# Kernel tuning notes

Hardware: AMD Instinct MI355X
Metric: run time of the kernel (lower is better)

## Reference

```python
import jax, jax.numpy as jnp
import numpy as np

GROUPS = 8
EPS = 1e-5
NUM_HEADS = 8


def group_norm(x, gamma, beta):
    # x: [B, C, N]; GroupNorm over (C//G, N) per group, per sample (torch semantics)
    B, C, N = x.shape
    xg = x.reshape(B, GROUPS, (C // GROUPS) * N)
    mean = xg.mean(axis=-1, keepdims=True)
    var = xg.var(axis=-1, keepdims=True)
    xn = ((xg - mean) * jax.lax.rsqrt(var + EPS)).reshape(B, C, N)
    return xn * gamma[None, :, None] + beta[None, :, None]


def setup_inputs() -> dict:
    key = jax.random.key(0)
    ks = jax.random.split(key, 6)
    B, N, C = 4, 2048, 512
    s = 0.02
    return {
        "x": jax.random.normal(ks[0], (B, N, C), jnp.float32),
        "pe": jax.random.normal(ks[1], (B, N, C), jnp.float32),
        "qkv_w": jax.random.normal(ks[2], (3 * C, C), jnp.float32) * s,
        "proj_w": jax.random.normal(ks[3], (C, C), jnp.float32) * s,
        "proj_b": jnp.zeros((C,), jnp.float32),
        "conv1_w": jax.random.normal(ks[4], (C, C), jnp.float32) * s,
        "conv1_b": jnp.zeros((C,), jnp.float32),
        "gn1_g": jnp.ones((C,), jnp.float32),
        "gn1_b": jnp.zeros((C,), jnp.float32),
        "conv2_w": jax.random.normal(ks[5], (C, C), jnp.float32) * s,
        "conv2_b": jnp.zeros((C,), jnp.float32),
        "gn2_g": jnp.ones((C,), jnp.float32),
        "gn2_b": jnp.zeros((C,), jnp.float32),
    }


def reference(x, pe, qkv_w, proj_w, proj_b, conv1_w, conv1_b, gn1_g, gn1_b,
              conv2_w, conv2_b, gn2_g, gn2_b):
    B, N, C = x.shape
    H = NUM_HEADS
    D = C // H
    scale = D ** -0.5

    pe_t = pe.transpose(0, 2, 1)  # [B, C, N]
    # Conv1d(kernel=1) == per-position linear over channels
    p1 = group_norm(jnp.einsum('oc,bcn->bon', conv1_w, pe_t) + conv1_b[None, :, None], gn1_g, gn1_b)
    p2 = group_norm(jnp.einsum('oc,bcn->bon', conv2_w, pe_t) + conv2_b[None, :, None], gn2_g, gn2_b)
    pe_1 = p1.transpose(0, 2, 1)                 # [B, N, C]
    pe_attn = jax.nn.sigmoid(jnp.einsum('bnc,bcm->bnm', pe_1, p2))  # [B, N, N]

    qkv = (x @ qkv_w.T).reshape(B, N, 3, H, D).transpose(2, 0, 3, 1, 4)  # [3, B, H, N, D]
    q, k, v = qkv[0], qkv[1], qkv[2]

    attn = jnp.einsum('bhnd,bhmd->bhnm', q, k) * scale
    attn = attn * pe_attn[:, None, :, :]
    attn = jax.nn.softmax(attn, axis=-1)

    out = jnp.einsum('bhnm,bhmd->bhnd', attn, v)          # [B, H, N, D]
    out = out.transpose(0, 2, 1, 3).reshape(B, N, C)
    return out @ proj_w.T + proj_b
```

## Files before the change

### kernel.cpp

```cpp
#include <hip/hip_runtime.h>
#include <hip/hip_bf16.h>

typedef __attribute__((ext_vector_type(8))) short bf16x8;
typedef __attribute__((ext_vector_type(4))) float f32x4;

__device__ __forceinline__ float bfu2f(unsigned int u) {
    return __uint_as_float(u << 16);
}
__device__ __forceinline__ unsigned short f2bfu(float f) {
    unsigned int u = __float_as_uint(f);
    u += 0x7fffu + ((u >> 16) & 1u);
    return (unsigned short)(u >> 16);
}

__global__ __launch_bounds__(256) void cvt2(const float* __restrict__ s0, unsigned short* __restrict__ d0,
                                            const float* __restrict__ s1, unsigned short* __restrict__ d1) {
    int i = blockIdx.x * 256 + threadIdx.x;
    const int stride = gridDim.x * 256;
    for (; i < 1048576; i += stride) {
        float4 v = reinterpret_cast<const float4*>(s0)[i];
        ushort4 o;
        o.x = f2bfu(v.x); o.y = f2bfu(v.y); o.z = f2bfu(v.z); o.w = f2bfu(v.w);
        reinterpret_cast<ushort4*>(d0)[i] = o;
        float4 u = reinterpret_cast<const float4*>(s1)[i];
        ushort4 p;
        p.x = f2bfu(u.x); p.y = f2bfu(u.y); p.z = f2bfu(u.z); p.w = f2bfu(u.w);
        reinterpret_cast<ushort4*>(d1)[i] = p;
    }
}

__global__ __launch_bounds__(256) void cvtw(const float* __restrict__ s0, unsigned short* __restrict__ d0,
                                            const float* __restrict__ s1, unsigned short* __restrict__ d1,
                                            const float* __restrict__ s2, unsigned short* __restrict__ d2,
                                            const float* __restrict__ s3, unsigned short* __restrict__ d3) {
    int i = blockIdx.x * 256 + threadIdx.x;
    const int stride = gridDim.x * 256;
    for (; i < 393216; i += stride) {
        const float* s; unsigned short* d; int j;
        if (i < 196608)      { s = s0; d = d0; j = i; }
        else if (i < 262144) { s = s1; d = d1; j = i - 196608; }
        else if (i < 327680) { s = s2; d = d2; j = i - 262144; }
        else                 { s = s3; d = d3; j = i - 327680; }
        float4 v = reinterpret_cast<const float4*>(s)[j];
        ushort4 o;
        o.x = f2bfu(v.x); o.y = f2bfu(v.y); o.z = f2bfu(v.z); o.w = f2bfu(v.w);
        reinterpret_cast<ushort4*>(d)[j] = o;
    }
}

template <int EPI>
__global__ __launch_bounds__(256) void gemm_nt(
    const unsigned short* __restrict__ A, const unsigned short* __restrict__ B,
    void* __restrict__ C0, void* __restrict__ C1, void* __restrict__ C2,
    const float* __restrict__ bias, int K, long sA, long sB, long sC) {
    __shared__ unsigned short As[2][128 * 32];
    __shared__ unsigned short Bs[2][128 * 32];
    const int tid = threadIdx.x;
    const int l = tid & 63, w = tid >> 6;
    const int wr = w >> 1, wc = w & 1, lr = l & 15, lh = l >> 4;
    const int m0 = blockIdx.y * 128, n0 = blockIdx.x * 128;
    A += (size_t)blockIdx.z * sA;
    B += (size_t)blockIdx.z * sB;
    f32x4 acc[4][4] = {};

    const int srow = l >> 2, sslot = l & 3;
    auto stage = [&](int bufi, int k0) {
#pragma unroll
        for (int i = 0; i < 2; i++) {
            const int row = w * 32 + i * 16 + srow;
            const int cs = (sslot ^ (row & 3)) * 8;
            const int ldsoff = (w * 32 + i * 16) * 32;
            __builtin_amdgcn_global_load_lds(
                (const __attribute__((address_space(1))) void*)(A + (size_t)(m0 + row) * K + k0 + cs),
                (__attribute__((address_space(3))) void*)&As[bufi][ldsoff], 16, 0, 0);
            __builtin_amdgcn_global_load_lds(
                (const __attribute__((address_space(1))) void*)(B + (size_t)(n0 + row) * K + k0 + cs),
                (__attribute__((address_space(3))) void*)&Bs[bufi][ldsoff], 16, 0, 0);
        }
    };

    const int nks = K >> 5;
    stage(0, 0);
    asm volatile("s_waitcnt vmcnt(0)" ::: "memory");
    __builtin_amdgcn_s_barrier();
    __builtin_amdgcn_sched_barrier(0);

    const int colA = (lh ^ (lr & 3)) << 3;
    for (int ks = 0; ks < nks; ks++) {
        const int cur = ks & 1;
        if (ks + 1 < nks) stage(cur ^ 1, (ks + 1) << 5);
        bf16x8 af[4], bfr[4];
#pragma unroll
        for (int i = 0; i < 4; i++)
            af[i] = *reinterpret_cast<const bf16x8*>(&As[cur][(wr * 64 + i * 16 + lr) * 32 + colA]);
#pragma unroll
        for (int i = 0; i < 4; i++)
            bfr[i] = *reinterpret_cast<const bf16x8*>(&Bs[cur][(wc * 64 + i * 16 + lr) * 32 + colA]);
        __builtin_amdgcn_s_setprio(1);
#pragma unroll
        for (int mi = 0; mi < 4; mi++)
#pragma unroll
            for (int ni = 0; ni < 4; ni++)
                acc[mi][ni] = __builtin_amdgcn_mfma_f32_16x16x32_bf16(af[mi], bfr[ni], acc[mi][ni], 0, 0, 0);
        __builtin_amdgcn_s_setprio(0);
        if (ks + 1 < nks) {
            asm volatile("s_waitcnt vmcnt(0) lgkmcnt(0)" ::: "memory");
            __builtin_amdgcn_s_barrier();
            __builtin_amdgcn_sched_barrier(0);
        }
    }

#pragma unroll
    for (int mi = 0; mi < 4; mi++) {
#pragma unroll
        for (int ni = 0; ni < 4; ni++) {
#pragma unroll
            for (int r = 0; r < 4; r++) {
                const int row = m0 + wr * 64 + mi * 16 + lh * 4 + r;
                const int col = n0 + wc * 64 + ni * 16 + lr;
                float v = acc[mi][ni][r];
                if constexpr (EPI == 0) {
                    v += bias[col];
                    ((unsigned short*)C0)[(size_t)row * 512 + col] = f2bfu(v);
                } else if constexpr (EPI == 1) {
                    const int part = col >> 9, hh = (col >> 6) & 7, d = col & 63;
                    const int b = row >> 11, n = row & 2047;
                    const size_t bh = (size_t)(b * 8 + hh);
                    if (part == 0)
                        ((unsigned short*)C0)[(bh * 2048 + n) * 64 + d] = f2bfu(v * 0.1803368801111244f);
                    else if (part == 1)
                        ((unsigned short*)C1)[(bh * 2048 + n) * 64 + d] = f2bfu(v);
                    else
                        ((unsigned short*)C2)[(bh * 64 + d) * 2048 + n] = f2bfu(v);
                } else if constexpr (EPI == 2) {
                    const float sg = 1.0f / (1.0f + __expf(-v));
                    ((unsigned short*)C0)[(size_t)blockIdx.z * sC + (size_t)row * 2048 + col] = f2bfu(sg);
                } else {
                    ((float*)C0)[(size_t)row * 512 + col] = v + bias[col];
                }
            }
        }
    }
}

__global__ __launch_bounds__(256) void gn_stats_part(const unsigned short* __restrict__ c1,
                                                     const unsigned short* __restrict__ c2,
                                                     float* __restrict__ part) {
    const int bgc = blockIdx.x;
    const int b = bgc >> 6, g = (bgc >> 3) & 7, ch = bgc & 7;
    const int tid = threadIdx.x;
    const size_t base = ((size_t)b * 2048 + ch * 256) * 512 + g * 64;
    float s1 = 0.f, q1 = 0.f, s2 = 0.f, q2 = 0.f;
    for (int c = tid; c < 2048; c += 256) {
        const int n = c >> 3, i8 = (c & 7) * 8;
        const size_t off = base + (size_t)n * 512 + i8;
        uint4 v1 = *reinterpret_cast<const uint4*>(c1 + off);
        uint4 v2 = *reinterpret_cast<const uint4*>(c2 + off);
        unsigned int a1[4] = {v1.x, v1.y, v1.z, v1.w};
        unsigned int a2[4] = {v2.x, v2.y, v2.z, v2.w};
#pragma unroll
        for (int j = 0; j < 4; j++) {
            float x0 = bfu2f(a1[j] & 0xffffu), x1 = bfu2f(a1[j] >> 16);
            s1 += x0 + x1; q1 += x0 * x0 + x1 * x1;
            float y0 = bfu2f(a2[j] & 0xffffu), y1 = bfu2f(a2[j] >> 16);
            s2 += y0 + y1; q2 += y0 * y0 + y1 * y1;
        }
    }
#pragma unroll
    for (int off = 32; off >= 1; off >>= 1) {
        s1 += __shfl_down(s1, off); q1 += __shfl_down(q1, off);
        s2 += __shfl_down(s2, off); q2 += __shfl_down(q2, off);
    }
    __shared__ float red[4][4];
    if ((tid & 63) == 0) {
        const int wv = tid >> 6;
        red[0][wv] = s1; red[1][wv] = q1; red[2][wv] = s2; red[3][wv] = q2;
    }
    __syncthreads();
    if (tid == 0) {
        part[bgc * 4 + 0] = red[0][0] + red[0][1] + red[0][2] + red[0][3];
        part[bgc * 4 + 1] = red[1][0] + red[1][1] + red[1][2] + red[1][3];
        part[bgc * 4 + 2] = red[2][0] + red[2][1] + red[2][2] + red[2][3];
        part[bgc * 4 + 3] = red[3][0] + red[3][1] + red[3][2] + red[3][3];
    }
}

__global__ __launch_bounds__(256) void gn_apply(unsigned short* __restrict__ c1,
                                                unsigned short* __restrict__ c2,
                                                const float* __restrict__ part,
                                                const float* __restrict__ g1, const float* __restrict__ b1,
                                                const float* __restrict__ g2, const float* __restrict__ b2) {
    __shared__ float sst[32][4];
    const int tid = threadIdx.x;
    if (tid < 32) {
        float S1 = 0.f, Q1 = 0.f, S2 = 0.f, Q2 = 0.f;
        for (int ch = 0; ch < 8; ch++) {
            const float* p = part + ((tid << 3) + ch) * 4;
            S1 += p[0]; Q1 += p[1]; S2 += p[2]; Q2 += p[3];
        }
        const float inv = 1.0f / 131072.0f;
        float m1 = S1 * inv, m2 = S2 * inv;
        float v1 = fmaxf(Q1 * inv - m1 * m1, 0.f);
        float v2 = fmaxf(Q2 * inv - m2 * m2, 0.f);
        sst[tid][0] = m1;
        sst[tid][1] = rsqrtf(v1 + 1e-5f);
        sst[tid][2] = m2;
        sst[tid][3] = rsqrtf(v2 + 1e-5f);
    }
    __syncthreads();
    int i = blockIdx.x * 256 + tid;
    const int stride = gridDim.x * 256;
    for (; i < 524288; i += stride) {
        const size_t e = (size_t)i * 8;
        const int b = (int)(e >> 20);
        const int o = (int)(e & 511);
        const int g = o >> 6;
        const float* st = sst[(b << 3) + g];
        const float m1 = st[0], r1 = st[1], m2 = st[2], r2 = st[3];
        uint4 v1 = *reinterpret_cast<const uint4*>(c1 + e);
        uint4 v2 = *reinterpret_cast<const uint4*>(c2 + e);
        unsigned int a1[4] = {v1.x, v1.y, v1.z, v1.w};
        unsigned int a2[4] = {v2.x, v2.y, v2.z, v2.w};
        unsigned int o1[4], o2[4];
#pragma unroll
        for (int j = 0; j < 4; j++) {
            const int oo = o + j * 2;
            float x0 = (bfu2f(a1[j] & 0xffffu) - m1) * r1 * g1[oo] + b1[oo];
            float x1 = (bfu2f(a1[j] >> 16) - m1) * r1 * g1[oo + 1] + b1[oo + 1];
            o1[j] = (unsigned int)f2bfu(x0) | ((unsigned int)f2bfu(x1) << 16);
            float y0 = (bfu2f(a2[j] & 0xffffu) - m2) * r2 * g2[oo] + b2[oo];
            float y1 = (bfu2f(a2[j] >> 16) - m2) * r2 * g2[oo + 1] + b2[oo + 1];
            o2[j] = (unsigned int)f2bfu(y0) | ((unsigned int)f2bfu(y1) << 16);
        }
        uint4 w1; w1.x = o1[0]; w1.y = o1[1]; w1.z = o1[2]; w1.w = o1[3];
        uint4 w2; w2.x = o2[0]; w2.y = o2[1]; w2.z = o2[2]; w2.w = o2[3];
        *reinterpret_cast<uint4*>(c1 + e) = w1;
        *reinterpret_cast<uint4*>(c2 + e) = w2;
    }
}

__global__ __launch_bounds__(256, 4) void attn_fused(
    const unsigned short* __restrict__ qb, const unsigned short* __restrict__ kb,
    const unsigned short* __restrict__ vT, const unsigned short* __restrict__ pea,
    unsigned short* __restrict__ hbuf) {
    __shared__ unsigned short Ks[2][64 * 64];
    __shared__ unsigned short Vs[2][64 * 64];
    __shared__ unsigned short Pl[4][16 * 64];
    const int tid = threadIdx.x, l = tid & 63, w = tid >> 6;
    const int lr = l & 15, lh = l >> 4;
    const int bid = blockIdx.x;
    const int h = bid >> 7, rst = bid & 127, nt = rst & 31, b = rst >> 5;
    const size_t bh = (size_t)(b * 8 + h);
    const unsigned short* qp = qb + bh * 2048 * 64;
    const unsigned short* kp = kb + bh * 2048 * 64;
    const unsigned short* vp = vT + bh * 64 * 2048;
    const unsigned short* pep = pea + (size_t)b * 2048 * 2048;
    const int n0 = nt * 64;

    bf16x8 qf[2];
    qf[0] = *reinterpret_cast<const bf16x8*>(qp + (size_t)(n0 + 16 * w + lr) * 64 + lh * 8);
    qf[1] = *reinterpret_cast<const bf16x8*>(qp + (size_t)(n0 + 16 * w + lr) * 64 + 32 + lh * 8);

    const int swz = (lr & 7) << 4;
    const int colK0 = ((16 * lh) ^ swz) >> 1;
    const int colK1 = ((64 + 16 * lh) ^ swz) >> 1;

    const unsigned short* perp = pep + (size_t)(n0 + 16 * w + lr) * 2048;
    uint2 peR[4];
#pragma unroll
    for (int mf = 0; mf < 4; mf++)
        peR[mf] = *reinterpret_cast<const uint2*>(perp + 16 * mf + 4 * lh);

    f32x4 oacc[4] = {};
    float mrun = -1e30f, lrun = 0.f;

    const int srow = l >> 3, sslot = l & 7;
    auto stage_kv = [&](int bufi, int m0) {
#pragma unroll
        for (int i = 0; i < 2; i++) {
            const int row = w * 16 + i * 8 + srow;
            const int cs = (sslot ^ (row & 7)) * 8;
            const int ldsoff = (w * 16 + i * 8) * 64;
            __builtin_amdgcn_global_load_lds(
                (const __attribute__((address_space(1))) void*)(kp + (size_t)(m0 + row) * 64 + cs),
                (__attribute__((address_space(3))) void*)&Ks[bufi][ldsoff], 16, 0, 0);
            __builtin_amdgcn_global_load_lds(
                (const __attribute__((address_space(1))) void*)(vp + (size_t)row * 2048 + m0 + cs),
                (__attribute__((address_space(3))) void*)&Vs[bufi][ldsoff], 16, 0, 0);
        }
    };

    stage_kv(0, 0);
    asm volatile("s_waitcnt vmcnt(0)" ::: "memory");
    __builtin_amdgcn_s_barrier();
    __builtin_amdgcn_sched_barrier(0);

    for (int mt = 0; mt < 32; mt++) {
        const int cur = mt & 1;
        if (mt + 1 < 32) stage_kv(cur ^ 1, (mt + 1) * 64);
        const unsigned short* Kb = Ks[cur];
        const unsigned short* Vb = Vs[cur];

        f32x4 st[4] = {};
        __builtin_amdgcn_s_setprio(1);
#pragma unroll
        for (int mf = 0; mf < 4; mf++) {
            bf16x8 kf0 = *reinterpret_cast<const bf16x8*>(&Kb[(mf * 16 + lr) * 64 + colK0]);
            bf16x8 kf1 = *reinterpret_cast<const bf16x8*>(&Kb[(mf * 16 + lr) * 64 + colK1]);
            st[mf] = __builtin_amdgcn_mfma_f32_16x16x32_bf16(kf0, qf[0], st[mf], 0, 0, 0);
            st[mf] = __builtin_amdgcn_mfma_f32_16x16x32_bf16(kf1, qf[1], st[mf], 0, 0, 0);
        }
        __builtin_amdgcn_s_setprio(0);

        float p[4][4];
#pragma unroll
        for (int mf = 0; mf < 4; mf++) {
            p[mf][0] = st[mf][0] * bfu2f(peR[mf].x & 0xffffu);
            p[mf][1] = st[mf][1] * bfu2f(peR[mf].x >> 16);
            p[mf][2] = st[mf][2] * bfu2f(peR[mf].y & 0xffffu);
            p[mf][3] = st[mf][3] * bfu2f(peR[mf].y >> 16);
        }
        uint2 peN[4];
        if (mt + 1 < 32) {
            const unsigned short* pn = perp + (mt + 1) * 64;
#pragma unroll
            for (int mf = 0; mf < 4; mf++)
                peN[mf] = *reinterpret_cast<const uint2*>(pn + 16 * mf + 4 * lh);
        }
        float pm = fmaxf(p[0][0], p[0][1]);
        pm = fmaxf(fmaxf(pm, p[0][2]), p[0][3]);
#pragma unroll
        for (int mf = 1; mf < 4; mf++) {
            pm = fmaxf(fmaxf(pm, p[mf][0]), p[mf][1]);
            pm = fmaxf(fmaxf(pm, p[mf][2]), p[mf][3]);
        }
        pm = fmaxf(pm, __shfl_xor(pm, 16));
        pm = fmaxf(pm, __shfl_xor(pm, 32));
        if (__any(pm > mrun + 11.5416f)) {
            const float mnew = fmaxf(mrun, pm);
            const float fac = __builtin_amdgcn_exp2f(mrun - mnew);
            lrun *= fac;
#pragma unroll
            for (int df = 0; df < 4; df++)
#pragma unroll
                for (int r = 0; r < 4; r++) oacc[df][r] *= fac;
            mrun = mnew;
        }
        float ss = 0.f;
        unsigned int pk[8];
#pragma unroll
        for (int mf = 0; mf < 4; mf++) {
#pragma unroll
            for (int t = 0; t < 2; t++) {
                const float a = __builtin_amdgcn_exp2f(p[mf][2 * t] - mrun);
                const float c = __builtin_amdgcn_exp2f(p[mf][2 * t + 1] - mrun);
                unsigned int pkv;
                asm("v_cvt_pk_bf16_f32 %0, %1, %2" : "=v"(pkv) : "v"(a), "v"(c));
                pk[mf * 2 + t] = pkv;
                ss += a + c;
            }
        }
        ss += __shfl_xor(ss, 16);
        ss += __shfl_xor(ss, 32);
        lrun += ss;
        unsigned short* PlW = Pl[w];
        const int plswz = (lr & 7) << 4;
#pragma unroll
        for (int mf = 0; mf < 4; mf++)
#pragma unroll
            for (int t = 0; t < 2; t++) {
                const int cb = (mf * 32 + lh * 8 + 4 * t) ^ plswz;
                *reinterpret_cast<unsigned int*>(&PlW[lr * 64 + (cb >> 1)]) = pk[mf * 2 + t];
            }
        bf16x8 pb0 = *reinterpret_cast<const bf16x8*>(&PlW[lr * 64 + (((lh * 16) ^ plswz) >> 1)]);
        bf16x8 pb1 = *reinterpret_cast<const bf16x8*>(&PlW[lr * 64 + (((64 + lh * 16) ^ plswz) >> 1)]);
        __builtin_amdgcn_s_setprio(1);
#pragma unroll
        for (int df = 0; df < 4; df++) {
            bf16x8 vf0 = *reinterpret_cast<const bf16x8*>(&Vb[(df * 16 + lr) * 64 + colK0]);
            bf16x8 vf1 = *reinterpret_cast<const bf16x8*>(&Vb[(df * 16 + lr) * 64 + colK1]);
            oacc[df] = __builtin_amdgcn_mfma_f32_16x16x32_bf16(vf0, pb0, oacc[df], 0, 0, 0);
            oacc[df] = __builtin_amdgcn_mfma_f32_16x16x32_bf16(vf1, pb1, oacc[df], 0, 0, 0);
        }
        __builtin_amdgcn_s_setprio(0);
        if (mt + 1 < 32) {
            asm volatile("s_waitcnt vmcnt(0) lgkmcnt(0)" ::: "memory");
            __builtin_amdgcn_s_barrier();
            __builtin_amdgcn_sched_barrier(0);
#pragma unroll
            for (int mf = 0; mf < 4; mf++) peR[mf] = peN[mf];
        }
    }
    const float inv = 1.0f / lrun;
    const size_t base = ((size_t)b * 2048 + n0 + 16 * w + lr) * 512 + h * 64;
#pragma unroll
    for (int df = 0; df < 4; df++) {
#pragma unroll
        for (int t = 0; t < 2; t++) {
            const unsigned int ua = f2bfu(oacc[df][2 * t] * inv);
            const unsigned int uc = f2bfu(oacc[df][2 * t + 1] * inv);
            *reinterpret_cast<unsigned int*>(&hbuf[base + 16 * df + 4 * lh + 2 * t]) = ua | (uc << 16);
        }
    }
}

extern "C" void kernel_launch(void* const* d_in, const int* in_sizes, int n_in,
                              void* d_out, int out_size, void* d_ws, size_t ws_size,
                              hipStream_t stream) {
    const float* x       = (const float*)d_in[0];
    const float* pe      = (const float*)d_in[1];
    const float* qkv_w   = (const float*)d_in[2];
    const float* proj_w  = (const float*)d_in[3];
    const float* proj_b  = (const float*)d_in[4];
    const float* conv1_w = (const float*)d_in[5];
    const float* conv1_b = (const float*)d_in[6];
    const float* gn1_g   = (const float*)d_in[7];
    const float* gn1_b   = (const float*)d_in[8];
    const float* conv2_w = (const float*)d_in[9];
    const float* conv2_b = (const float*)d_in[10];
    const float* gn2_g   = (const float*)d_in[11];
    const float* gn2_b   = (const float*)d_in[12];
    float* out = (float*)d_out;

    char* ws = (char*)d_ws;
    size_t off = 0;
    auto alloc = [&](size_t bytes) -> void* {
        void* p = ws + off;
        off += (bytes + 255) & ~(size_t)255;
        return p;
    };
    unsigned short* xb     = (unsigned short*)alloc(8388608);
    unsigned short* peb    = (unsigned short*)alloc(8388608);
    unsigned short* qkvwb  = (unsigned short*)alloc(1572864);
    unsigned short* projwb = (unsigned short*)alloc(524288);
    unsigned short* w1b    = (unsigned short*)alloc(524288);
    unsigned short* w2b    = (unsigned short*)alloc(524288);
    unsigned short* c1b    = (unsigned short*)alloc(8388608);
    unsigned short* c2b    = (unsigned short*)alloc(8388608);
    unsigned short* qbuf   = (unsigned short*)alloc(8388608);
    unsigned short* kbuf   = (unsigned short*)alloc(8388608);
    unsigned short* vtb    = (unsigned short*)alloc(8388608);
    unsigned short* peatt  = (unsigned short*)alloc(33554432);
    unsigned short* hbuf   = (unsigned short*)alloc(8388608);
    float* part            = (float*)alloc(4096);

    dim3 blk(256);
    cvt2<<<1024, blk, 0, stream>>>(x, xb, pe, peb);
    cvtw<<<512, blk, 0, stream>>>(qkv_w, qkvwb, proj_w, projwb, conv1_w, w1b, conv2_w, w2b);

    gemm_nt<0><<<dim3(4, 64, 1), blk, 0, stream>>>(peb, w1b, c1b, nullptr, nullptr, conv1_b, 512, 0, 0, 0);
    gemm_nt<0><<<dim3(4, 64, 1), blk, 0, stream>>>(peb, w2b, c2b, nullptr, nullptr, conv2_b, 512, 0, 0, 0);
    gn_stats_part<<<256, blk, 0, stream>>>(c1b, c2b, part);
    gn_apply<<<1024, blk, 0, stream>>>(c1b, c2b, part, gn1_g, gn1_b, gn2_g, gn2_b);
    gemm_nt<1><<<dim3(12, 64, 1), blk, 0, stream>>>(xb, qkvwb, qbuf, kbuf, vtb, nullptr, 512, 0, 0, 0);
    gemm_nt<2><<<dim3(16, 16, 4), blk, 0, stream>>>(c1b, c2b, peatt, nullptr, nullptr, nullptr, 512,
                                                    1048576, 1048576, 4194304);
    attn_fused<<<dim3(1024, 1, 1), blk, 0, stream>>>(qbuf, kbuf, vtb, peatt, hbuf);
    gemm_nt<3><<<dim3(4, 64, 1), blk, 0, stream>>>(hbuf, projwb, out, nullptr, nullptr, proj_b, 512, 0, 0, 0);
}
```

Before: 232.5 us.

## Fuse conversion kernels, batch conv GEMMs, and compute GroupNorm stats in epilogue

Merges the activation and weight fp32-to-bf16 conversion kernels into one launch that also packs both conv biases into a contiguous workspace. The two conv1/conv2 GEMMs become a single launch using blockIdx.z, with the weights assumed adjacent in the workspace so sB=262144 selects the second. Each wave accumulates GroupNorm sum and sum-of-squares in the epilogue and atomically adds them into a zeroed buffer, which removes the separate stats pass over c1/c2. The cost is a memset, float atomics with nondeterministic summation order, and statistics taken from fp32 values before bf16 rounding.

Result: no change. 228.6 us (-1.7%).

```diff
diff --git a/kernel.cpp b/kernel.cpp
--- a/kernel.cpp
+++ b/kernel.cpp
@@ -13,38 +13,44 @@
     return (unsigned short)(u >> 16);
 }
 
-__global__ __launch_bounds__(256) void cvt2(const float* __restrict__ s0, unsigned short* __restrict__ d0,
-                                            const float* __restrict__ s1, unsigned short* __restrict__ d1) {
-    int i = blockIdx.x * 256 + threadIdx.x;
+__global__ __launch_bounds__(256) void cvt_all(
+    const float* __restrict__ x, unsigned short* __restrict__ xb,
+    const float* __restrict__ pe, unsigned short* __restrict__ peb,
+    const float* __restrict__ w0, unsigned short* __restrict__ d0,
+    const float* __restrict__ w1, unsigned short* __restrict__ d1,
+    const float* __restrict__ w2, unsigned short* __restrict__ d2,
+    const float* __restrict__ w3, unsigned short* __restrict__ d3,
+    const float* __restrict__ c1bias, const float* __restrict__ c2bias,
+    float* __restrict__ biasws) {
+    const int tid = threadIdx.x;
+    if (blockIdx.x == 0) {
+        if (tid < 128) ((float4*)biasws)[tid] = ((const float4*)c1bias)[tid];
+        else ((float4*)biasws)[tid] = ((const float4*)c2bias)[tid - 128];
+    }
+    int i = blockIdx.x * 256 + tid;
     const int stride = gridDim.x * 256;
-    for (; i < 1048576; i += stride) {
-        float4 v = reinterpret_cast<const float4*>(s0)[i];
-        ushort4 o;
-        o.x = f2bfu(v.x); o.y = f2bfu(v.y); o.z = f2bfu(v.z); o.w = f2bfu(v.w);
-        reinterpret_cast<ushort4*>(d0)[i] = o;
-        float4 u = reinterpret_cast<const float4*>(s1)[i];
-        ushort4 p;
-        p.x = f2bfu(u.x); p.y = f2bfu(u.y); p.z = f2bfu(u.z); p.w = f2bfu(u.w);
-        reinterpret_cast<ushort4*>(d1)[i] = p;
-    }
-}
-
-__global__ __launch_bounds__(256) void cvtw(const float* __restrict__ s0, unsigned short* __restrict__ d0,
-                                            const float* __restrict__ s1, unsigned short* __restrict__ d1,
-                                            const float* __restrict__ s2, unsigned short* __restrict__ d2,
-                                            const float* __restrict__ s3, unsigned short* __restrict__ d3) {
-    int i = blockIdx.x * 256 + threadIdx.x;
-    const int stride = gridDim.x * 256;
-    for (; i < 393216; i += stride) {
-        const float* s; unsigned short* d; int j;
-        if (i < 196608)      { s = s0; d = d0; j = i; }
-        else if (i < 262144) { s = s1; d = d1; j = i - 196608; }
-        else if (i < 327680) { s = s2; d = d2; j = i - 262144; }
-        else                 { s = s3; d = d3; j = i - 327680; }
-        float4 v = reinterpret_cast<const float4*>(s)[j];
-        ushort4 o;
-        o.x = f2bfu(v.x); o.y = f2bfu(v.y); o.z = f2bfu(v.z); o.w = f2bfu(v.w);
-        reinterpret_cast<ushort4*>(d)[j] = o;
+    for (; i < 1441792; i += stride) {
+        if (i < 1048576) {
+            float4 v = reinterpret_cast<const float4*>(x)[i];
+            ushort4 o;
+            o.x = f2bfu(v.x); o.y = f2bfu(v.y); o.z = f2bfu(v.z); o.w = f2bfu(v.w);
+            reinterpret_cast<ushort4*>(xb)[i] = o;
+            float4 u = reinterpret_cast<const float4*>(pe)[i];
+            ushort4 p;
+            p.x = f2bfu(u.x); p.y = f2bfu(u.y); p.z = f2bfu(u.z); p.w = f2bfu(u.w);
+            reinterpret_cast<ushort4*>(peb)[i] = p;
+        } else {
+            int j = i - 1048576;
+            const float* s; unsigned short* d;
+            if (j < 196608)      { s = w0; d = d0; }
+            else if (j < 262144) { s = w1; d = d1; j -= 196608; }
+            else if (j < 327680) { s = w2; d = d2; j -= 262144; }
+            else                 { s = w3; d = d3; j -= 327680; }
+            float4 v = reinterpret_cast<const float4*>(s)[j];
+            ushort4 o;
+            o.x = f2bfu(v.x); o.y = f2bfu(v.y); o.z = f2bfu(v.z); o.w = f2bfu(v.w);
+            reinterpret_cast<ushort4*>(d)[j] = o;
+        }
     }
 }
 
@@ -110,6 +116,7 @@
         }
     }
 
+    float sgn = 0.f, qgn = 0.f;
 #pragma unroll
     for (int mi = 0; mi < 4; mi++) {
 #pragma unroll
@@ -120,8 +127,9 @@
                 const int col = n0 + wc * 64 + ni * 16 + lr;
                 float v = acc[mi][ni][r];
                 if constexpr (EPI == 0) {
-                    v += bias[col];
-                    ((unsigned short*)C0)[(size_t)row * 512 + col] = f2bfu(v);
+                    v += bias[blockIdx.z * 512 + col];
+                    sgn += v; qgn += v * v;
+                    ((unsigned short*)C0)[(size_t)blockIdx.z * sC + (size_t)row * 512 + col] = f2bfu(v);
                 } else if constexpr (EPI == 1) {
                     const int part = col >> 9, hh = (col >> 6) & 7, d = col & 63;
                     const int b = row >> 11, n = row & 2047;
@@ -141,47 +149,18 @@
             }
         }
     }
-}
-
-__global__ __launch_bounds__(256) void gn_stats_part(const unsigned short* __restrict__ c1,
-                                                     const unsigned short* __restrict__ c2,
-                                                     float* __restrict__ part) {
-    const int bgc = blockIdx.x;
-    const int b = bgc >> 6, g = (bgc >> 3) & 7, ch = bgc & 7;
-    const int tid = threadIdx.x;
-    const size_t base = ((size_t)b * 2048 + ch * 256) * 512 + g * 64;
-    float s1 = 0.f, q1 = 0.f, s2 = 0.f, q2 = 0.f;
-    for (int c = tid; c < 2048; c += 256) {
-        const int n = c >> 3, i8 = (c & 7) * 8;
-        const size_t off = base + (size_t)n * 512 + i8;
-        uint4 v1 = *reinterpret_cast<const uint4*>(c1 + off);
-        uint4 v2 = *reinterpret_cast<const uint4*>(c2 + off);
-        unsigned int a1[4] = {v1.x, v1.y, v1.z, v1.w};
-        unsigned int a2[4] = {v2.x, v2.y, v2.z, v2.w};
-#pragma unroll
-        for (int j = 0; j < 4; j++) {
-            float x0 = bfu2f(a1[j] & 0xffffu), x1 = bfu2f(a1[j] >> 16);
-            s1 += x0 + x1; q1 += x0 * x0 + x1 * x1;
-            float y0 = bfu2f(a2[j] & 0xffffu), y1 = bfu2f(a2[j] >> 16);
-            s2 += y0 + y1; q2 += y0 * y0 + y1 * y1;
-        }
-    }
-#pragma unroll
-    for (int off = 32; off >= 1; off >>= 1) {
-        s1 += __shfl_down(s1, off); q1 += __shfl_down(q1, off);
-        s2 += __shfl_down(s2, off); q2 += __shfl_down(q2, off);
-    }
-    __shared__ float red[4][4];
-    if ((tid & 63) == 0) {
-        const int wv = tid >> 6;
-        red[0][wv] = s1; red[1][wv] = q1; red[2][wv] = s2; red[3][wv] = q2;
-    }
-    __syncthreads();
-    if (tid == 0) {
-        part[bgc * 4 + 0] = red[0][0] + red[0][1] + red[0][2] + red[0][3];
-        part[bgc * 4 + 1] = red[1][0] + red[1][1] + red[1][2] + red[1][3];
-        part[bgc * 4 + 2] = red[2][0] + red[2][1] + red[2][2] + red[2][3];
-        part[bgc * 4 + 3] = red[3][0] + red[3][1] + red[3][2] + red[3][3];
+    if constexpr (EPI == 0) {
+#pragma unroll
+        for (int s = 1; s < 64; s <<= 1) {
+            sgn += __shfl_xor(sgn, s);
+            qgn += __shfl_xor(qgn, s);
+        }
+        if (l == 0) {
+            const int bg = ((blockIdx.y >> 4) << 3) + blockIdx.x * 2 + wc;
+            float* part = (float*)C1;
+            atomicAdd(&part[(blockIdx.z * 32 + bg) * 2 + 0], sgn);
+            atomicAdd(&part[(blockIdx.z * 32 + bg) * 2 + 1], qgn);
+        }
     }
 }
 
@@ -190,22 +169,17 @@
                                                 const float* __restrict__ part,
                                                 const float* __restrict__ g1, const float* __restrict__ b1,
                                                 const float* __restrict__ g2, const float* __restrict__ b2) {
-    __shared__ float sst[32][4];
+    __shared__ float sst[2][32][2];
     const int tid = threadIdx.x;
-    if (tid < 32) {
-        float S1 = 0.f, Q1 = 0.f, S2 = 0.f, Q2 = 0.f;
-        for (int ch = 0; ch < 8; ch++) {
-            const float* p = part + ((tid << 3) + ch) * 4;
-            S1 += p[0]; Q1 += p[1]; S2 += p[2]; Q2 += p[3];
-        }
+    if (tid < 64) {
+        const int z = tid >> 5, bg = tid & 31;
+        const float S = part[(z * 32 + bg) * 2 + 0];
+        const float Q = part[(z * 32 + bg) * 2 + 1];
         const float inv = 1.0f / 131072.0f;
-        float m1 = S1 * inv, m2 = S2 * inv;
-        float v1 = fmaxf(Q1 * inv - m1 * m1, 0.f);
-        float v2 = fmaxf(Q2 * inv - m2 * m2, 0.f);
-        sst[tid][0] = m1;
-        sst[tid][1] = rsqrtf(v1 + 1e-5f);
-        sst[tid][2] = m2;
-        sst[tid][3] = rsqrtf(v2 + 1e-5f);
+        const float m = S * inv;
+        const float v = fmaxf(Q * inv - m * m, 0.f);
+        sst[z][bg][0] = m;
+        sst[z][bg][1] = rsqrtf(v + 1e-5f);
     }
     __syncthreads();
     int i = blockIdx.x * 256 + tid;
@@ -215,8 +189,9 @@
         const int b = (int)(e >> 20);
         const int o = (int)(e & 511);
         const int g = o >> 6;
-        const float* st = sst[(b << 3) + g];
-        const float m1 = st[0], r1 = st[1], m2 = st[2], r2 = st[3];
+        const int bg = (b << 3) + g;
+        const float m1 = sst[0][bg][0], r1 = sst[0][bg][1];
+        const float m2 = sst[1][bg][0], r2 = sst[1][bg][1];
         uint4 v1 = *reinterpret_cast<const uint4*>(c1 + e);
         uint4 v2 = *reinterpret_cast<const uint4*>(c2 + e);
         unsigned int a1[4] = {v1.x, v1.y, v1.z, v1.w};
@@ -442,15 +417,16 @@
     unsigned short* vtb    = (unsigned short*)alloc(8388608);
     unsigned short* peatt  = (unsigned short*)alloc(33554432);
     unsigned short* hbuf   = (unsigned short*)alloc(8388608);
-    float* part            = (float*)alloc(4096);
+    float* part            = (float*)alloc(512);
+    float* biasws          = (float*)alloc(4096);
 
     dim3 blk(256);
-    cvt2<<<1024, blk, 0, stream>>>(x, xb, pe, peb);
-    cvtw<<<512, blk, 0, stream>>>(qkv_w, qkvwb, proj_w, projwb, conv1_w, w1b, conv2_w, w2b);
-
-    gemm_nt<0><<<dim3(4, 64, 1), blk, 0, stream>>>(peb, w1b, c1b, nullptr, nullptr, conv1_b, 512, 0, 0, 0);
-    gemm_nt<0><<<dim3(4, 64, 1), blk, 0, stream>>>(peb, w2b, c2b, nullptr, nullptr, conv2_b, 512, 0, 0, 0);
-    gn_stats_part<<<256, blk, 0, stream>>>(c1b, c2b, part);
+    hipMemsetAsync(part, 0, 512, stream);
+    cvt_all<<<2048, blk, 0, stream>>>(x, xb, pe, peb, qkv_w, qkvwb, proj_w, projwb,
+                                      conv1_w, w1b, conv2_w, w2b, conv1_b, conv2_b, biasws);
+
+    gemm_nt<0><<<dim3(4, 64, 2), blk, 0, stream>>>(peb, w1b, c1b, part, nullptr, biasws,
+                                                   512, 0, 262144, 4194304);
     gn_apply<<<1024, blk, 0, stream>>>(c1b, c2b, part, gn1_g, gn1_b, gn2_g, gn2_b);
     gemm_nt<1><<<dim3(12, 64, 1), blk, 0, stream>>>(xb, qkvwb, qbuf, kbuf, vtb, nullptr, 512, 0, 0, 0);
     gemm_nt<2><<<dim3(16, 16, 4), blk, 0, stream>>>(c1b, c2b, peatt, nullptr, nullptr, nullptr, 512,
```
